# Kernel tuning notes

Hardware: AMD Instinct MI355X
Metric: run time of the kernel (lower is better)

## Reference

```python
import jax, jax.numpy as jnp
import numpy as np

L = 10      # LSTM layers
H = 128     # hidden size
ENC = 4096  # traffic_encoder_output_len
B = 8192    # batch
T = 12      # points_to_predict
NUM_MODES = 25


def setup_inputs() -> dict:
    key = jax.random.key(0)
    ks = jax.random.split(key, 10)
    s = 1.0 / np.sqrt(H)
    return {
        "backbone_encoded": jax.random.normal(ks[0], (B, ENC), jnp.float32),
        "fc_in_W": jax.random.normal(ks[1], (H, ENC), jnp.float32) / np.sqrt(ENC),
        "fc_in_b": jax.random.normal(ks[2], (H,), jnp.float32) * s,
        "Wih": jax.random.normal(ks[3], (L, 4 * H, H), jnp.float32) * s,
        "Whh": jax.random.normal(ks[4], (L, 4 * H, H), jnp.float32) * s,
        "bih": jax.random.normal(ks[5], (L, 4 * H), jnp.float32) * s,
        "bhh": jax.random.normal(ks[6], (L, 4 * H), jnp.float32) * s,
        "fc_out_W": jax.random.normal(ks[7], (3 * NUM_MODES, H), jnp.float32) * s,
        "fc_out_b": jax.random.normal(ks[8], (3 * NUM_MODES,), jnp.float32) * s,
        "points_to_predict": T,
    }


def _lstm_stack(x, Wih, Whh, bih, bhh):
    # x: [B, T, H]; PyTorch gate order: i, f, g, o
    def run_layer(x, l):
        def step(carry, xt):
            h, c = carry
            gates = xt @ Wih[l].T + h @ Whh[l].T + bih[l] + bhh[l]  # [B, 4H]
            i, f, g, o = jnp.split(gates, 4, axis=-1)
            c = jax.nn.sigmoid(f) * c + jax.nn.sigmoid(i) * jnp.tanh(g)
            h = jax.nn.sigmoid(o) * jnp.tanh(c)
            return (h, c), h
        b = x.shape[0]
        h0 = jnp.zeros((b, H), x.dtype)
        _, ys = jax.lax.scan(step, (h0, h0), jnp.swapaxes(x, 0, 1))  # [T, B, H]
        return jnp.swapaxes(ys, 0, 1)

    for l in range(L):
        x = run_layer(x, l)
    return x


def reference(backbone_encoded, fc_in_W, fc_in_b, Wih, Whh, bih, bhh,
              fc_out_W, fc_out_b, points_to_predict):
    enc = jax.nn.relu(backbone_encoded @ fc_in_W.T + fc_in_b)        # [B, H]
    x = jnp.repeat(enc[:, None, :], points_to_predict, axis=1)      # [B, T, H]
    y = _lstm_stack(x, Wih, Whh, bih, bhh)                           # [B, T, H]
    fc = y @ fc_out_W.T + fc_out_b                                   # [B, T, 75]
    b, t, _ = fc.shape
    # chunk(25, dim=channels) of consecutive pairs -> [B, 25, T, 2]
    predictions = fc[:, :, :50].reshape(b, t, NUM_MODES, 2).transpose(0, 2, 1, 3)
    probabilities = jax.nn.softmax(fc[:, -1, 50:], axis=-1)          # [B, 25]
    return predictions, probabilities
```

## Files before the change

kernel.cpp:

```cpp
#include <hip/hip_runtime.h>

typedef _Float16 h16;
typedef _Float16 h8 __attribute__((ext_vector_type(8)));
typedef float f4 __attribute__((ext_vector_type(4)));

#define NB 8192
#define NENC 4096
#define NH 128
#define NL 10
#define NT 12

#define OFF_FCIN 0
#define SZ_FCIN (128*4096)
#define OFF_W (OFF_FCIN + SZ_FCIN)
#define SZ_W (10*2*512*128)
#define OFF_FCOUT (OFF_W + SZ_W)
#define SZ_FCOUT (80*128)
#define OFF_ENC (OFF_FCOUT + SZ_FCOUT)
#define SZ_ENC (8192*128)
#define BYTE_BIAS ((OFF_ENC + SZ_ENC)*2)

__device__ __forceinline__ float sigf(float x) {
  float e = __builtin_amdgcn_exp2f(-1.4426950408889634f * x);
  return __builtin_amdgcn_rcpf(1.0f + e);
}
__device__ __forceinline__ float tanhf_(float x) {
  float e = __builtin_amdgcn_exp2f(-2.8853900817779268f * x);
  return 2.0f * __builtin_amdgcn_rcpf(1.0f + e) - 1.0f;
}
__device__ __forceinline__ f4 splat4(float v) { f4 r; r[0]=v; r[1]=v; r[2]=v; r[3]=v; return r; }

__device__ __forceinline__ int packidx(int r, int k, int Kd8) {
  return ((r >> 4) * Kd8 + (k >> 3)) * 128 + ((r & 15) << 3) + (k & 7);
}

__global__ __launch_bounds__(256) void prep(const float* __restrict__ fcinW,
                                            const float* __restrict__ Wih,
                                            const float* __restrict__ Whh,
                                            const float* __restrict__ bih,
                                            const float* __restrict__ bhh,
                                            const float* __restrict__ fcoutW,
                                            h16* __restrict__ wsh,
                                            float* __restrict__ wbias) {
  int idx = blockIdx.x * 256 + threadIdx.x;
  if (idx < 524288) {
    int r = idx >> 12, k = idx & 4095;
    wsh[OFF_FCIN + packidx(r, k, 512)] = (h16)fcinW[idx];
  } else if (idx < 524288 + 1310720) {
    int rel = idx - 524288;
    int l = rel / 131072; int rr = rel % 131072;
    int ssel = rr >> 16; int rk = rr & 65535;
    int r = rk >> 7, k = rk & 127;
    float v = ssel ? Whh[l * 65536 + rk] : Wih[l * 65536 + rk];
    wsh[OFF_W + (l * 2 + ssel) * 65536 + packidx(r, k, 16)] = (h16)v;
  } else if (idx < 524288 + 1310720 + 10240) {
    int rel = idx - (524288 + 1310720);
    int r = rel >> 7, k = rel & 127;
    float v = (r < 75) ? fcoutW[r * 128 + k] : 0.0f;
    wsh[OFF_FCOUT + packidx(r, k, 16)] = (h16)v;
  } else if (idx < 524288 + 1310720 + 10240 + 5120) {
    int rel = idx - (524288 + 1310720 + 10240);
    wbias[rel] = bih[rel] + bhh[rel];
  }
}

__global__ __launch_bounds__(256) void kin(const float* __restrict__ A,
                                           const float* __restrict__ bvec,
                                           h16* __restrict__ wsh) {
  const h16* Wp = wsh + OFF_FCIN;
  h16* ench = wsh + OFF_ENC;
  int tid = threadIdx.x;
  int w = tid >> 6, lane = tid & 63, s = lane & 15, q = lane >> 4;
  int m0 = blockIdx.x * 16;
  int c0 = w * 32 + s, c1 = c0 + 16;
  f4 acc0 = splat4(bvec[c0]);
  f4 acc1 = splat4(bvec[c1]);
  const float* arow = A + (size_t)(m0 + s) * NENC;
  const h16* wp0 = Wp + (w * 2 + 0) * (512 * 128) + s * 8;
  const h16* wp1 = Wp + (w * 2 + 1) * (512 * 128) + s * 8;
#pragma unroll 4
  for (int kb = 0; kb < 128; ++kb) {
    int k0 = kb * 32 + q * 8;
    float4 x0 = *(const float4*)(arow + k0);
    float4 x1 = *(const float4*)(arow + k0 + 4);
    h8 af;
    af[0] = (h16)x0.x; af[1] = (h16)x0.y; af[2] = (h16)x0.z; af[3] = (h16)x0.w;
    af[4] = (h16)x1.x; af[5] = (h16)x1.y; af[6] = (h16)x1.z; af[7] = (h16)x1.w;
    h8 b0 = *(const h8*)(wp0 + (kb * 4 + q) * 128);
    h8 b1 = *(const h8*)(wp1 + (kb * 4 + q) * 128);
    acc0 = __builtin_amdgcn_mfma_f32_16x16x32_f16(af, b0, acc0, 0, 0, 0);
    acc1 = __builtin_amdgcn_mfma_f32_16x16x32_f16(af, b1, acc1, 0, 0, 0);
  }
#pragma unroll
  for (int r = 0; r < 4; ++r) {
    int b = m0 + q * 4 + r;
    float v0 = acc0[r]; v0 = v0 > 0.f ? v0 : 0.f;
    float v1 = acc1[r]; v1 = v1 > 0.f ? v1 : 0.f;
    ench[(size_t)b * NH + c0] = (h16)v0;
    ench[(size_t)b * NH + c1] = (h16)v1;
  }
}

__global__ __launch_bounds__(256, 1) void lstm(h16* __restrict__ wsh,
                                               const float* __restrict__ wbias,
                                               const float* __restrict__ fcoutb,
                                               float* __restrict__ out) {
  __shared__ h16 xbuf[NT][32][136];
  __shared__ h16 hbuf[2][32][136];
  int tid = threadIdx.x;
  int w = tid >> 6, lane = tid & 63, s = lane & 15, q = lane >> 4;
  int brow = blockIdx.x * 32;
  const h16* ench = wsh + OFF_ENC;
  {
    int r = tid >> 3, cg = (tid & 7) * 16;
    h8 e0 = *(const h8*)(ench + (size_t)(brow + r) * NH + cg);
    h8 e1 = *(const h8*)(ench + (size_t)(brow + r) * NH + cg + 8);
    for (int t = 0; t < NT; ++t) {
      *(h8*)&xbuf[t][r][cg] = e0;
      *(h8*)&xbuf[t][r][cg + 8] = e1;
    }
  }
  h8 wx[4][2][4], wh[4][2][4];
  float bb[4][2];
  float c[2][2][4];
  for (int l = 0; l < NL; ++l) {
    const h16* wih = wsh + OFF_W + (l * 2 + 0) * 65536;
    const h16* whh = wsh + OFF_W + (l * 2 + 1) * 65536;
#pragma unroll
    for (int g = 0; g < 4; ++g)
#pragma unroll
      for (int uc = 0; uc < 2; ++uc) {
        int rb = g * 8 + w * 2 + uc;
#pragma unroll
        for (int kt = 0; kt < 4; ++kt) {
          int off = (rb * 16 + kt * 4 + q) * 128 + s * 8;
          wx[g][uc][kt] = *(const h8*)(wih + off);
          wh[g][uc][kt] = *(const h8*)(whh + off);
        }
        bb[g][uc] = wbias[l * 512 + g * 128 + w * 32 + uc * 16 + s];
      }
#pragma unroll
    for (int mt = 0; mt < 2; ++mt)
#pragma unroll
      for (int uc = 0; uc < 2; ++uc)
#pragma unroll
        for (int r = 0; r < 4; ++r) c[mt][uc][r] = 0.f;
    for (int j = tid; j < 32 * 136; j += 256) hbuf[0][0][j] = (h16)0.f;
    __syncthreads();
    for (int t = 0; t < NT; ++t) {
      int cur = t & 1, nxt = cur ^ 1;
      h8 ax[2][4], ah[2][4];
#pragma unroll
      for (int mt = 0; mt < 2; ++mt)
#pragma unroll
        for (int kt = 0; kt < 4; ++kt) {
          ax[mt][kt] = *(const h8*)&xbuf[t][mt * 16 + s][kt * 32 + q * 8];
          ah[mt][kt] = *(const h8*)&hbuf[cur][mt * 16 + s][kt * 32 + q * 8];
        }
      __syncthreads();
#pragma unroll
      for (int mt = 0; mt < 2; ++mt) {
        f4 acc[4][2];
#pragma unroll
        for (int g = 0; g < 4; ++g)
#pragma unroll
          for (int uc = 0; uc < 2; ++uc) {
            f4 a = splat4(bb[g][uc]);
#pragma unroll
            for (int kt = 0; kt < 4; ++kt) {
              a = __builtin_amdgcn_mfma_f32_16x16x32_f16(ax[mt][kt], wx[g][uc][kt], a, 0, 0, 0);
              a = __builtin_amdgcn_mfma_f32_16x16x32_f16(ah[mt][kt], wh[g][uc][kt], a, 0, 0, 0);
            }
            acc[g][uc] = a;
          }
#pragma unroll
        for (int uc = 0; uc < 2; ++uc)
#pragma unroll
          for (int r = 0; r < 4; ++r) {
            float iv = acc[0][uc][r], fv = acc[1][uc][r];
            float gv = acc[2][uc][r], ov = acc[3][uc][r];
            float cc = sigf(fv) * c[mt][uc][r] + sigf(iv) * tanhf_(gv);
            c[mt][uc][r] = cc;
            float hv = sigf(ov) * tanhf_(cc);
            int row = mt * 16 + q * 4 + r, col = w * 32 + uc * 16 + s;
            h16 hx = (h16)hv;
            hbuf[nxt][row][col] = hx;
            xbuf[t][row][col] = hx;
          }
      }
      __syncthreads();
    }
  }
  h8 wo[5][4];
  float bo[5];
  const h16* fco = wsh + OFF_FCOUT;
#pragma unroll
  for (int nt = 0; nt < 5; ++nt) {
#pragma unroll
    for (int kt = 0; kt < 4; ++kt)
      wo[nt][kt] = *(const h8*)(fco + (nt * 16 + kt * 4 + q) * 128 + s * 8);
    int col = nt * 16 + s;
    bo[nt] = (col < 75) ? fcoutb[col] : 0.f;
  }
  float* probst = (float*)&hbuf[0][0][0];
  for (int tt = 0; tt < 3; ++tt) {
    int t = w * 3 + tt;
    h8 ax[2][4];
#pragma unroll
    for (int mt = 0; mt < 2; ++mt)
#pragma unroll
      for (int kt = 0; kt < 4; ++kt)
        ax[mt][kt] = *(const h8*)&xbuf[t][mt * 16 + s][kt * 32 + q * 8];
#pragma unroll
    for (int mt = 0; mt < 2; ++mt)
#pragma unroll
      for (int nt = 0; nt < 5; ++nt) {
        f4 a = splat4(bo[nt]);
#pragma unroll
        for (int kt = 0; kt < 4; ++kt)
          a = __builtin_amdgcn_mfma_f32_16x16x32_f16(ax[mt][kt], wo[nt][kt], a, 0, 0, 0);
        int col = nt * 16 + s;
#pragma unroll
        for (int r = 0; r < 4; ++r) {
          int row = mt * 16 + q * 4 + r;
          int b = brow + row;
          float v = a[r];
          if (col < 50)
            out[(size_t)b * 600 + (col >> 1) * 24 + t * 2 + (col & 1)] = v;
          if (t == 11 && col >= 50 && col < 75)
            probst[row * 26 + (col - 50)] = v;
        }
      }
  }
  __syncthreads();
  if (tid < 32) {
    float vals[25];
    float m = -1e30f;
#pragma unroll
    for (int j = 0; j < 25; ++j) { vals[j] = probst[tid * 26 + j]; m = vals[j] > m ? vals[j] : m; }
    float sum = 0.f;
#pragma unroll
    for (int j = 0; j < 25; ++j) {
      float e = __builtin_amdgcn_exp2f((vals[j] - m) * 1.4426950408889634f);
      vals[j] = e; sum += e;
    }
    float rs = 1.0f / sum;
    size_t pb = (size_t)4915200 + (size_t)(brow + tid) * 25;
#pragma unroll
    for (int j = 0; j < 25; ++j) out[pb + j] = vals[j] * rs;
  }
}

extern "C" void kernel_launch(void* const* d_in, const int* in_sizes, int n_in,
                              void* d_out, int out_size, void* d_ws, size_t ws_size,
                              hipStream_t stream) {
  const float* backbone = (const float*)d_in[0];
  const float* fcinW    = (const float*)d_in[1];
  const float* fcinb    = (const float*)d_in[2];
  const float* Wih      = (const float*)d_in[3];
  const float* Whh      = (const float*)d_in[4];
  const float* bih      = (const float*)d_in[5];
  const float* bhh      = (const float*)d_in[6];
  const float* fcoutW   = (const float*)d_in[7];
  const float* fcoutb   = (const float*)d_in[8];
  h16* wsh = (h16*)d_ws;
  float* wbias = (float*)((char*)d_ws + BYTE_BIAS);

  prep<<<7228, 256, 0, stream>>>(fcinW, Wih, Whh, bih, bhh, fcoutW, wsh, wbias);
  kin<<<512, 256, 0, stream>>>(backbone, fcinb, wsh);
  lstm<<<256, 256, 0, stream>>>(wsh, wbias, fcoutb, (float*)d_out);
}
```

Before: 617.4 us.

## Split LSTM gate columns across 8 waves and vectorize weight prep

The LSTM kernel now runs 512 threads per block, 8 waves each owning 16 hidden columns instead of 4 waves owning 32. This halves per-thread register weights and doubles wave-level parallelism for the serial recurrence. The h write-back is moved after a barrier so all waves finish reading before overwrite. The prep kernel also converts 8 floats per thread with vector loads and stores instead of scalar scattered writes. The cost is more barrier participants and the 256-block grid still only fills part of the GPU.

```diff
diff --git a/kernel.cpp b/kernel.cpp
--- a/kernel.cpp
+++ b/kernel.cpp
@@ -29,9 +29,9 @@
   return 2.0f * __builtin_amdgcn_rcpf(1.0f + e) - 1.0f;
 }
 __device__ __forceinline__ f4 splat4(float v) { f4 r; r[0]=v; r[1]=v; r[2]=v; r[3]=v; return r; }
-
-__device__ __forceinline__ int packidx(int r, int k, int Kd8) {
-  return ((r >> 4) * Kd8 + (k >> 3)) * 128 + ((r & 15) << 3) + (k & 7);
+__device__ __forceinline__ h8 cvt8(float4 a, float4 b) {
+  h8 r; r[0]=(h16)a.x; r[1]=(h16)a.y; r[2]=(h16)a.z; r[3]=(h16)a.w;
+  r[4]=(h16)b.x; r[5]=(h16)b.y; r[6]=(h16)b.z; r[7]=(h16)b.w; return r;
 }
 
 __global__ __launch_bounds__(256) void prep(const float* __restrict__ fcinW,
@@ -43,23 +43,33 @@
                                             h16* __restrict__ wsh,
                                             float* __restrict__ wbias) {
   int idx = blockIdx.x * 256 + threadIdx.x;
-  if (idx < 524288) {
-    int r = idx >> 12, k = idx & 4095;
-    wsh[OFF_FCIN + packidx(r, k, 512)] = (h16)fcinW[idx];
-  } else if (idx < 524288 + 1310720) {
-    int rel = idx - 524288;
-    int l = rel / 131072; int rr = rel % 131072;
-    int ssel = rr >> 16; int rk = rr & 65535;
-    int r = rk >> 7, k = rk & 127;
-    float v = ssel ? Whh[l * 65536 + rk] : Wih[l * 65536 + rk];
-    wsh[OFF_W + (l * 2 + ssel) * 65536 + packidx(r, k, 16)] = (h16)v;
-  } else if (idx < 524288 + 1310720 + 10240) {
-    int rel = idx - (524288 + 1310720);
-    int r = rel >> 7, k = rel & 127;
-    float v = (r < 75) ? fcoutW[r * 128 + k] : 0.0f;
-    wsh[OFF_FCOUT + packidx(r, k, 16)] = (h16)v;
-  } else if (idx < 524288 + 1310720 + 10240 + 5120) {
-    int rel = idx - (524288 + 1310720 + 10240);
+  if (idx < 65536) {
+    int r = idx >> 9, k8 = idx & 511;
+    const float* src = fcinW + r * 4096 + k8 * 8;
+    h8 v = cvt8(*(const float4*)src, *(const float4*)(src + 4));
+    *(h8*)(wsh + OFF_FCIN + (((r >> 4) * 512 + k8) * 128 + (r & 15) * 8)) = v;
+  } else if (idx < 229376) {
+    int rel = idx - 65536;
+    int l = rel >> 14, rr = rel & 16383;
+    int ssel = rr >> 13, rk8 = rr & 8191;
+    int r = rk8 >> 4, k8 = rk8 & 15;
+    const float* src = (ssel ? Whh : Wih) + l * 65536 + r * 128 + k8 * 8;
+    h8 v = cvt8(*(const float4*)src, *(const float4*)(src + 4));
+    *(h8*)(wsh + OFF_W + (l * 2 + ssel) * 65536 +
+           (((r >> 4) * 16 + k8) * 128 + (r & 15) * 8)) = v;
+  } else if (idx < 230656) {
+    int rel = idx - 229376;
+    int r = rel >> 4, k8 = rel & 15;
+    h8 v;
+    if (r < 75) {
+      const float* src = fcoutW + r * 128 + k8 * 8;
+      v = cvt8(*(const float4*)src, *(const float4*)(src + 4));
+    } else {
+      for (int j = 0; j < 8; ++j) v[j] = (h16)0.f;
+    }
+    *(h8*)(wsh + OFF_FCOUT + (((r >> 4) * 16 + k8) * 128 + (r & 15) * 8)) = v;
+  } else if (idx < 235776) {
+    int rel = idx - 230656;
     wbias[rel] = bih[rel] + bhh[rel];
   }
 }
@@ -83,9 +93,7 @@
     int k0 = kb * 32 + q * 8;
     float4 x0 = *(const float4*)(arow + k0);
     float4 x1 = *(const float4*)(arow + k0 + 4);
-    h8 af;
-    af[0] = (h16)x0.x; af[1] = (h16)x0.y; af[2] = (h16)x0.z; af[3] = (h16)x0.w;
-    af[4] = (h16)x1.x; af[5] = (h16)x1.y; af[6] = (h16)x1.z; af[7] = (h16)x1.w;
+    h8 af = cvt8(x0, x1);
     h8 b0 = *(const h8*)(wp0 + (kb * 4 + q) * 128);
     h8 b1 = *(const h8*)(wp1 + (kb * 4 + q) * 128);
     acc0 = __builtin_amdgcn_mfma_f32_16x16x32_f16(af, b0, acc0, 0, 0, 0);
@@ -101,7 +109,7 @@
   }
 }
 
-__global__ __launch_bounds__(256, 1) void lstm(h16* __restrict__ wsh,
+__global__ __launch_bounds__(512, 2) void lstm(h16* __restrict__ wsh,
                                                const float* __restrict__ wbias,
                                                const float* __restrict__ fcoutb,
                                                float* __restrict__ out) {
@@ -112,82 +120,76 @@
   int brow = blockIdx.x * 32;
   const h16* ench = wsh + OFF_ENC;
   {
-    int r = tid >> 3, cg = (tid & 7) * 16;
-    h8 e0 = *(const h8*)(ench + (size_t)(brow + r) * NH + cg);
-    h8 e1 = *(const h8*)(ench + (size_t)(brow + r) * NH + cg + 8);
-    for (int t = 0; t < NT; ++t) {
-      *(h8*)&xbuf[t][r][cg] = e0;
-      *(h8*)&xbuf[t][r][cg + 8] = e1;
-    }
-  }
-  h8 wx[4][2][4], wh[4][2][4];
-  float bb[4][2];
-  float c[2][2][4];
+    int r = tid >> 4, cg = (tid & 15) * 8;
+    h8 e = *(const h8*)(ench + (size_t)(brow + r) * NH + cg);
+#pragma unroll
+    for (int t = 0; t < NT; ++t) *(h8*)&xbuf[t][r][cg] = e;
+  }
+  h8 wx[4][4], wh[4][4];
+  float bb[4];
+  float c[2][4];
   for (int l = 0; l < NL; ++l) {
     const h16* wih = wsh + OFF_W + (l * 2 + 0) * 65536;
     const h16* whh = wsh + OFF_W + (l * 2 + 1) * 65536;
 #pragma unroll
-    for (int g = 0; g < 4; ++g)
-#pragma unroll
-      for (int uc = 0; uc < 2; ++uc) {
-        int rb = g * 8 + w * 2 + uc;
-#pragma unroll
-        for (int kt = 0; kt < 4; ++kt) {
-          int off = (rb * 16 + kt * 4 + q) * 128 + s * 8;
-          wx[g][uc][kt] = *(const h8*)(wih + off);
-          wh[g][uc][kt] = *(const h8*)(whh + off);
-        }
-        bb[g][uc] = wbias[l * 512 + g * 128 + w * 32 + uc * 16 + s];
+    for (int g = 0; g < 4; ++g) {
+#pragma unroll
+      for (int kt = 0; kt < 4; ++kt) {
+        int off = (((g * 8 + w) * 16 + kt * 4 + q) * 128) + s * 8;
+        wx[g][kt] = *(const h8*)(wih + off);
+        wh[g][kt] = *(const h8*)(whh + off);
       }
+      bb[g] = wbias[l * 512 + g * 128 + w * 16 + s];
+    }
 #pragma unroll
     for (int mt = 0; mt < 2; ++mt)
 #pragma unroll
-      for (int uc = 0; uc < 2; ++uc)
-#pragma unroll
-        for (int r = 0; r < 4; ++r) c[mt][uc][r] = 0.f;
-    for (int j = tid; j < 32 * 136; j += 256) hbuf[0][0][j] = (h16)0.f;
+      for (int r = 0; r < 4; ++r) c[mt][r] = 0.f;
+    for (int j = tid; j < 32 * 136 / 2; j += 512) ((unsigned int*)hbuf)[j] = 0u;
     __syncthreads();
     for (int t = 0; t < NT; ++t) {
       int cur = t & 1, nxt = cur ^ 1;
-      h8 ax[2][4], ah[2][4];
-#pragma unroll
-      for (int mt = 0; mt < 2; ++mt)
+      f4 acc[4][2];
+#pragma unroll
+      for (int g = 0; g < 4; ++g)
+#pragma unroll
+        for (int mt = 0; mt < 2; ++mt) acc[g][mt] = splat4(bb[g]);
+#pragma unroll
+      for (int mt = 0; mt < 2; ++mt) {
+        h8 ax[4], ah[4];
 #pragma unroll
         for (int kt = 0; kt < 4; ++kt) {
-          ax[mt][kt] = *(const h8*)&xbuf[t][mt * 16 + s][kt * 32 + q * 8];
-          ah[mt][kt] = *(const h8*)&hbuf[cur][mt * 16 + s][kt * 32 + q * 8];
-        }
-      __syncthreads();
-#pragma unroll
-      for (int mt = 0; mt < 2; ++mt) {
-        f4 acc[4][2];
+          ax[kt] = *(const h8*)&xbuf[t][mt * 16 + s][kt * 32 + q * 8];
+          ah[kt] = *(const h8*)&hbuf[cur][mt * 16 + s][kt * 32 + q * 8];
+        }
 #pragma unroll
         for (int g = 0; g < 4; ++g)
 #pragma unroll
-          for (int uc = 0; uc < 2; ++uc) {
-            f4 a = splat4(bb[g][uc]);
-#pragma unroll
-            for (int kt = 0; kt < 4; ++kt) {
-              a = __builtin_amdgcn_mfma_f32_16x16x32_f16(ax[mt][kt], wx[g][uc][kt], a, 0, 0, 0);
-              a = __builtin_amdgcn_mfma_f32_16x16x32_f16(ah[mt][kt], wh[g][uc][kt], a, 0, 0, 0);
-            }
-            acc[g][uc] = a;
-          }
-#pragma unroll
-        for (int uc = 0; uc < 2; ++uc)
-#pragma unroll
-          for (int r = 0; r < 4; ++r) {
-            float iv = acc[0][uc][r], fv = acc[1][uc][r];
-            float gv = acc[2][uc][r], ov = acc[3][uc][r];
-            float cc = sigf(fv) * c[mt][uc][r] + sigf(iv) * tanhf_(gv);
-            c[mt][uc][r] = cc;
-            float hv = sigf(ov) * tanhf_(cc);
-            int row = mt * 16 + q * 4 + r, col = w * 32 + uc * 16 + s;
-            h16 hx = (h16)hv;
-            hbuf[nxt][row][col] = hx;
-            xbuf[t][row][col] = hx;
+          for (int kt = 0; kt < 4; ++kt) {
+            acc[g][mt] = __builtin_amdgcn_mfma_f32_16x16x32_f16(ax[kt], wx[g][kt], acc[g][mt], 0, 0, 0);
+            acc[g][mt] = __builtin_amdgcn_mfma_f32_16x16x32_f16(ah[kt], wh[g][kt], acc[g][mt], 0, 0, 0);
           }
       }
+      h16 hv[2][4];
+#pragma unroll
+      for (int mt = 0; mt < 2; ++mt)
+#pragma unroll
+        for (int r = 0; r < 4; ++r) {
+          float iv = acc[0][mt][r], fv = acc[1][mt][r];
+          float gv = acc[2][mt][r], ov = acc[3][mt][r];
+          float cc = sigf(fv) * c[mt][r] + sigf(iv) * tanhf_(gv);
+          c[mt][r] = cc;
+          hv[mt][r] = (h16)(sigf(ov) * tanhf_(cc));
+        }
+      __syncthreads();
+#pragma unroll
+      for (int mt = 0; mt < 2; ++mt)
+#pragma unroll
+        for (int r = 0; r < 4; ++r) {
+          int row = mt * 16 + q * 4 + r, col = w * 16 + s;
+          xbuf[t][row][col] = hv[mt][r];
+          hbuf[nxt][row][col] = hv[mt][r];
+        }
       __syncthreads();
     }
   }
@@ -203,22 +205,21 @@
     bo[nt] = (col < 75) ? fcoutb[col] : 0.f;
   }
   float* probst = (float*)&hbuf[0][0][0];
-  for (int tt = 0; tt < 3; ++tt) {
-    int t = w * 3 + tt;
-    h8 ax[2][4];
-#pragma unroll
-    for (int mt = 0; mt < 2; ++mt)
+  int tcount = (w < 4) ? 2 : 1;
+  for (int ti = 0; ti < tcount; ++ti) {
+    int t = w + ti * 8;
+#pragma unroll
+    for (int mt = 0; mt < 2; ++mt) {
+      h8 ax[4];
 #pragma unroll
       for (int kt = 0; kt < 4; ++kt)
-        ax[mt][kt] = *(const h8*)&xbuf[t][mt * 16 + s][kt * 32 + q * 8];
-#pragma unroll
-    for (int mt = 0; mt < 2; ++mt)
+        ax[kt] = *(const h8*)&xbuf[t][mt * 16 + s][kt * 32 + q * 8];
 #pragma unroll
       for (int nt = 0; nt < 5; ++nt) {
         f4 a = splat4(bo[nt]);
 #pragma unroll
         for (int kt = 0; kt < 4; ++kt)
-          a = __builtin_amdgcn_mfma_f32_16x16x32_f16(ax[mt][kt], wo[nt][kt], a, 0, 0, 0);
+          a = __builtin_amdgcn_mfma_f32_16x16x32_f16(ax[kt], wo[nt][kt], a, 0, 0, 0);
         int col = nt * 16 + s;
 #pragma unroll
         for (int r = 0; r < 4; ++r) {
@@ -231,6 +232,7 @@
             probst[row * 26 + (col - 50)] = v;
         }
       }
+    }
   }
   __syncthreads();
   if (tid < 32) {
@@ -266,7 +268,7 @@
   h16* wsh = (h16*)d_ws;
   float* wbias = (float*)((char*)d_ws + BYTE_BIAS);
 
-  prep<<<7228, 256, 0, stream>>>(fcinW, Wih, Whh, bih, bhh, fcoutW, wsh, wbias);
+  prep<<<922, 256, 0, stream>>>(fcinW, Wih, Whh, bih, bhh, fcoutW, wsh, wbias);
   kin<<<512, 256, 0, stream>>>(backbone, fcinb, wsh);
-  lstm<<<256, 256, 0, stream>>>(wsh, wbias, fcoutb, (float*)d_out);
-}
+  lstm<<<256, 512, 0, stream>>>(wsh, wbias, fcoutb, (float*)d_out);
+}
```

After: 541.6 us. 1.14x faster.
